# Kernel optimization log

Hardware: AMD Instinct MI355X
Metric: run time of the kernel (lower is better)

The kernel has to match this reference:

```python
import jax, jax.numpy as jnp
import numpy as np

B, L, D = 4096, 50, 64
NU, NI, NR = 100000, 100000, 5


def setup_inputs() -> dict:
    key = jax.random.key(0)
    ks = jax.random.split(key, 16)
    s = 0.02
    inp = {
        "nodes_v": jax.random.randint(ks[0], (B,), 0, NI),
        "neigh_u": jax.random.randint(ks[1], (B, L), 0, NU),
        "neigh_r": jax.random.randint(ks[2], (B, L), 0, NR),
        "embed_u": jax.random.normal(ks[3], (NU, D)) * s,
        "embed_i": jax.random.normal(ks[4], (NI, D)) * s,
        "embed_r": jax.random.normal(ks[5], (NR, D)) * s,
        # gv MLP: Linear(2D,D) ReLU Linear(D,D) ReLU Linear(D,D)
        "gv_w1": jax.random.normal(ks[6], (2 * D, D)) * s, "gv_b1": jnp.zeros((D,)),
        "gv_w2": jax.random.normal(ks[7], (D, D)) * s,     "gv_b2": jnp.zeros((D,)),
        "gv_w3": jax.random.normal(ks[8], (D, D)) * s,     "gv_b3": jnp.zeros((D,)),
        # attention MLP: Linear(2D,D) ReLU Linear(D,D) ReLU Linear(D,1), softmax over neighbors
        "att_w1": jax.random.normal(ks[9], (2 * D, D)) * s, "att_b1": jnp.zeros((D,)),
        "att_w2": jax.random.normal(ks[10], (D, D)) * s,    "att_b2": jnp.zeros((D,)),
        "att_w3": jax.random.normal(ks[11], (D, 1)) * s,    "att_b3": jnp.zeros((1,)),
        # combine: Linear(2D,D) ReLU Linear(D,D) ReLU
        "wr1_w": jax.random.normal(ks[12], (2 * D, D)) * s, "wr1_b": jnp.zeros((D,)),
        "wr2_w": jax.random.normal(ks[13], (D, D)) * s,     "wr2_b": jnp.zeros((D,)),
    }
    return inp


def reference(nodes_v, neigh_u, neigh_r, embed_u, embed_i, embed_r,
              gv_w1, gv_b1, gv_w2, gv_b2, gv_w3, gv_b3,
              att_w1, att_b1, att_w2, att_b2, att_w3, att_b3,
              wr1_w, wr1_b, wr2_w, wr2_b):
    qj = embed_i[nodes_v]            # [B, D] item reps
    pt = embed_u[neigh_u]            # [B, L, D] neighbor user reps
    er = embed_r[neigh_r]            # [B, L, D] rating reps
    # fusion MLP g(.)
    x = jnp.concatenate([pt, er], axis=-1)                    # [B, L, 2D]
    h = jax.nn.relu(x @ gv_w1 + gv_b1)
    h = jax.nn.relu(h @ gv_w2 + gv_b2)
    fjt = h @ gv_w3 + gv_b3                                   # [B, L, D]
    # attention over neighbors (dropout is identity in eval mode)
    q_rep = jnp.broadcast_to(qj[:, None, :], fjt.shape)       # [B, L, D]
    a = jnp.concatenate([fjt, q_rep], axis=-1)                # [B, L, 2D]
    a = jax.nn.relu(a @ att_w1 + att_b1)
    a = jax.nn.relu(a @ att_w2 + att_b2)
    scores = (a @ att_w3 + att_b3)[..., 0]                    # [B, L]
    mu = jax.nn.softmax(scores, axis=1)                       # softmax over neighbors
    zj = jnp.einsum("bld,bl->bd", fjt, mu)                   # weighted aggregation
    # combine aggregated neighborhood with item's own embedding (2D -> D)
    z = jax.nn.relu(jnp.concatenate([zj, qj], axis=-1) @ wr1_w + wr1_b)
    out = jax.nn.relu(z @ wr2_w + wr2_b)                      # [B, D]
    return out
```

## Files before the change

kernel.cpp:

```cpp
#include <hip/hip_runtime.h>

typedef __bf16 bf16;
typedef short s16x8 __attribute__((ext_vector_type(8)));
typedef __bf16 b16x8 __attribute__((ext_vector_type(8)));
typedef float f32x4 __attribute__((ext_vector_type(4)));

#define B_   4096
#define L_   50
#define NROW (B_ * L_)
#define SX   136

#define OFF_W1T  0
#define OFF_W2T  8192
#define OFF_W3T  12288
#define OFF_WCA  16384
#define OFF_A2T  20480
#define OFF_R1T  24576
#define OFF_R2T  32768
#define WT_TOTAL 36864
#define BIAS1P_BYTE 73728
#define C_BYTE      73984
#define SC_BYTE     1122560
#define FJ_BYTE     1941760

__device__ __forceinline__ unsigned short f2b(float f) {
    __bf16 h = (__bf16)f;
    return __builtin_bit_cast(unsigned short, h);
}
__device__ __forceinline__ unsigned pack2(float a, float b) {
    return (unsigned)f2b(a) | ((unsigned)f2b(b) << 16);
}
__device__ __forceinline__ int div50(int x) {
    return (int)(((unsigned long long)(unsigned)x * 2748779070ull) >> 37);
}

template<int KT, bool RELU>
__device__ __forceinline__ void dual_layer(const bf16* A0, const bf16* A1,
                                           const bf16* Wp, const float* __restrict__ bias,
                                           bf16* O0, bf16* O1, int lane)
{
    const int m = lane & 15, quad = lane >> 4;
    f32x4 ac0[4] = {}, ac1[4] = {};
#pragma unroll
    for (int kt = 0; kt < KT; ++kt) {
        s16x8 a0 = *(const s16x8*)(A0 + m * SX + kt * 32 + quad * 8);
        s16x8 a1 = *(const s16x8*)(A1 + m * SX + kt * 32 + quad * 8);
#pragma unroll
        for (int nt = 0; nt < 4; ++nt) {
            s16x8 b = *(const s16x8*)(Wp + (nt * 16 + m) * (KT * 32) + kt * 32 + quad * 8);
            ac0[nt] = __builtin_amdgcn_mfma_f32_16x16x32_bf16(a0, b, ac0[nt], 0, 0, 0);
            ac1[nt] = __builtin_amdgcn_mfma_f32_16x16x32_bf16(a1, b, ac1[nt], 0, 0, 0);
        }
    }
#pragma unroll
    for (int nt = 0; nt < 4; ++nt) {
        int c = nt * 16 + m;
        float bv = bias[c];
#pragma unroll
        for (int r4 = 0; r4 < 4; ++r4) {
            float v0 = ac0[nt][r4] + bv, v1 = ac1[nt][r4] + bv;
            if (RELU) { v0 = fmaxf(v0, 0.f); v1 = fmaxf(v1, 0.f); }
            O0[(quad * 4 + r4) * SX + c] = (bf16)v0;
            O1[(quad * 4 + r4) * SX + c] = (bf16)v1;
        }
    }
}

extern "C" __global__ void prep_weights(const float* __restrict__ w1, const float* __restrict__ w2,
                                        const float* __restrict__ w3, const float* __restrict__ a1,
                                        const float* __restrict__ a2, const float* __restrict__ r1,
                                        const float* __restrict__ r2, const float* __restrict__ gb3,
                                        const float* __restrict__ ab1,
                                        bf16* __restrict__ wt, float* __restrict__ bias1p)
{
    int i = blockIdx.x * blockDim.x + threadIdx.x;
    if (i >= WT_TOTAL + 64) return;
    if (i >= WT_TOTAL) {
        int n = i - WT_TOTAL;
        float s0 = ab1[n], s1 = 0.f, s2 = 0.f, s3 = 0.f;
#pragma unroll
        for (int t = 0; t < 64; t += 4) {
            s0 = fmaf(gb3[t],     a1[t * 64 + n],       s0);
            s1 = fmaf(gb3[t + 1], a1[(t + 1) * 64 + n], s1);
            s2 = fmaf(gb3[t + 2], a1[(t + 2) * 64 + n], s2);
            s3 = fmaf(gb3[t + 3], a1[(t + 3) * 64 + n], s3);
        }
        bias1p[n] = (s0 + s1) + (s2 + s3);
        return;
    }
    float val;
    if (i < OFF_W2T)      { int li = i;            int n = li >> 7, k = li & 127; val = w1[k * 64 + n]; }
    else if (i < OFF_W3T) { int li = i - OFF_W2T;  int n = li >> 6, k = li & 63;  val = w2[k * 64 + n]; }
    else if (i < OFF_WCA) { int li = i - OFF_W3T;  int n = li >> 6, k = li & 63;  val = w3[k * 64 + n]; }
    else if (i < OFF_A2T) {
        int li = i - OFF_WCA; int n = li >> 6, k = li & 63;
        float s0 = 0.f, s1 = 0.f, s2 = 0.f, s3 = 0.f;
#pragma unroll
        for (int t = 0; t < 64; t += 4) {
            float4 w = *(const float4*)(w3 + k * 64 + t);
            s0 = fmaf(w.x, a1[t * 64 + n],       s0);
            s1 = fmaf(w.y, a1[(t + 1) * 64 + n], s1);
            s2 = fmaf(w.z, a1[(t + 2) * 64 + n], s2);
            s3 = fmaf(w.w, a1[(t + 3) * 64 + n], s3);
        }
        val = (s0 + s1) + (s2 + s3);
    }
    else if (i < OFF_R1T) { int li = i - OFF_A2T;  int n = li >> 6, k = li & 63;  val = a2[k * 64 + n]; }
    else if (i < OFF_R2T) { int li = i - OFF_R1T;  int n = li >> 7, k = li & 127; val = r1[k * 64 + n]; }
    else                  { int li = i - OFF_R2T;  int n = li >> 6, k = li & 63;  val = r2[k * 64 + n]; }
    wt[i] = (bf16)val;
}

extern "C" __global__ void __launch_bounds__(256, 4)
prep_citem(const int* __restrict__ nodes_v, const float* __restrict__ embed_i,
           const float* __restrict__ a1, const float* __restrict__ bias1p,
           float* __restrict__ cft)
{
    int gid = blockIdx.x * blockDim.x + threadIdx.x;
    int b = gid >> 6, n = gid & 63;
    int v = nodes_v[b];
    const float* q = embed_i + v * 64;
    float s0 = bias1p[n], s1 = 0.f, s2 = 0.f, s3 = 0.f;
#pragma unroll
    for (int k = 0; k < 64; k += 4) {
        s0 = fmaf(q[k],     a1[(64 + k) * 64 + n],     s0);
        s1 = fmaf(q[k + 1], a1[(64 + k + 1) * 64 + n], s1);
        s2 = fmaf(q[k + 2], a1[(64 + k + 2) * 64 + n], s2);
        s3 = fmaf(q[k + 3], a1[(64 + k + 3) * 64 + n], s3);
    }
    cft[gid] = (s0 + s1) + (s2 + s3);
}

extern "C" __global__ void __launch_bounds__(256, 2)
dense_fwd(const int* __restrict__ neigh_u, const int* __restrict__ neigh_r,
          const float* __restrict__ embed_u, const float* __restrict__ embed_r,
          const float* __restrict__ gv_b1, const float* __restrict__ gv_b2,
          const float* __restrict__ gv_b3,
          const float* __restrict__ att_b2, const float* __restrict__ att_w3,
          const bf16* __restrict__ wt, const float* __restrict__ cft,
          bf16* __restrict__ fj, float* __restrict__ scg)
{
    __shared__ __align__(16) bf16 Xs[128 * SX];
    __shared__ __align__(16) bf16 Ws[16384];
    __shared__ float csS[4 * 64];

    const int tid = threadIdx.x;
    const int lane = tid & 63, wave = tid >> 6;
    const int m = lane & 15, quad = lane >> 4;
    const int r0 = blockIdx.x * 128;
    const int b0 = div50(r0);

    {
        const uint4* src = (const uint4*)(wt + OFF_W2T);
        uint4* dst = (uint4*)Ws;
#pragma unroll
        for (int it = 0; it < 8; ++it) dst[tid + it * 256] = src[tid + it * 256];
    }
    {
        int i = tid >> 6, n = tid & 63;
        int bi = b0 + i; if (bi > B_ - 1) bi = B_ - 1;
        csS[tid] = cft[bi * 64 + n];
    }

    const int rw0 = wave * 32;
    {
        const int rsub = lane >> 4;
        const int c = lane & 15;
#pragma unroll
        for (int it = 0; it < 8; ++it) {
            int rloc = rw0 + it * 4 + rsub;
            int rg = r0 + rloc;
            int u = neigh_u[rg];
            int r = neigh_r[rg];
            float4 vu = *(const float4*)(embed_u + u * 64 + c * 4);
            float4 vr = *(const float4*)(embed_r + r * 64 + c * 4);
            uint2 pu, pr;
            pu.x = pack2(vu.x, vu.y); pu.y = pack2(vu.z, vu.w);
            pr.x = pack2(vr.x, vr.y); pr.y = pack2(vr.z, vr.w);
            *(uint2*)(Xs + rloc * SX + c * 4) = pu;
            *(uint2*)(Xs + rloc * SX + 64 + c * 4) = pr;
        }
    }

    bf16* X0 = Xs + rw0 * SX;
    bf16* X1 = Xs + (rw0 + 16) * SX;

    dual_layer<4, true>(X0, X1, wt + OFF_W1T, gv_b1, X0 + 64, X1 + 64, lane);

    __syncthreads();

    dual_layer<2, true>(X0 + 64, X1 + 64, Ws, gv_b2, X0, X1, lane);

    {
        const bf16* w3s = Ws + 4096;
        const bf16* wcs = Ws + 8192;
        f32x4 aF0[4] = {}, aF1[4] = {}, aA0[4] = {}, aA1[4] = {};
#pragma unroll
        for (int kt = 0; kt < 2; ++kt) {
            s16x8 a0 = *(const s16x8*)(X0 + m * SX + kt * 32 + quad * 8);
            s16x8 a1 = *(const s16x8*)(X1 + m * SX + kt * 32 + quad * 8);
#pragma unroll
            for (int nt = 0; nt < 4; ++nt) {
                s16x8 bF = *(const s16x8*)(w3s + (nt * 16 + m) * 64 + kt * 32 + quad * 8);
                s16x8 bA = *(const s16x8*)(wcs + (nt * 16 + m) * 64 + kt * 32 + quad * 8);
                aF0[nt] = __builtin_amdgcn_mfma_f32_16x16x32_bf16(a0, bF, aF0[nt], 0, 0, 0);
                aF1[nt] = __builtin_amdgcn_mfma_f32_16x16x32_bf16(a1, bF, aF1[nt], 0, 0, 0);
                aA0[nt] = __builtin_amdgcn_mfma_f32_16x16x32_bf16(a0, bA, aA0[nt], 0, 0, 0);
                aA1[nt] = __builtin_amdgcn_mfma_f32_16x16x32_bf16(a1, bA, aA1[nt], 0, 0, 0);
            }
        }
#pragma unroll
        for (int nt = 0; nt < 4; ++nt) {
            int c = nt * 16 + m;
            float b3v = gv_b3[c];
#pragma unroll
            for (int r4 = 0; r4 < 4; ++r4) {
                int rl0 = rw0 + quad * 4 + r4, rl1 = rl0 + 16;
                int i0 = div50(r0 + rl0) - b0, i1 = div50(r0 + rl1) - b0;
                Xs[rl0 * SX + 64 + c] = (bf16)(aF0[nt][r4] + b3v);
                Xs[rl1 * SX + 64 + c] = (bf16)(aF1[nt][r4] + b3v);
                Xs[rl0 * SX + c] = (bf16)fmaxf(aA0[nt][r4] + csS[i0 * 64 + c], 0.f);
                Xs[rl1 * SX + c] = (bf16)fmaxf(aA1[nt][r4] + csS[i1 * 64 + c], 0.f);
            }
        }
    }

    {
        const bf16* a2s = Ws + 12288;
        f32x4 ac0[4] = {}, ac1[4] = {};
#pragma unroll
        for (int kt = 0; kt < 2; ++kt) {
            s16x8 a0 = *(const s16x8*)(X0 + m * SX + kt * 32 + quad * 8);
            s16x8 a1 = *(const s16x8*)(X1 + m * SX + kt * 32 + quad * 8);
#pragma unroll
            for (int nt = 0; nt < 4; ++nt) {
                s16x8 b = *(const s16x8*)(a2s + (nt * 16 + m) * 64 + kt * 32 + quad * 8);
                ac0[nt] = __builtin_amdgcn_mfma_f32_16x16x32_bf16(a0, b, ac0[nt], 0, 0, 0);
                ac1[nt] = __builtin_amdgcn_mfma_f32_16x16x32_bf16(a1, b, ac1[nt], 0, 0, 0);
            }
        }
        float s0[4] = {0.f, 0.f, 0.f, 0.f}, s1[4] = {0.f, 0.f, 0.f, 0.f};
#pragma unroll
        for (int nt = 0; nt < 4; ++nt) {
            int c = nt * 16 + m;
            float b2v = att_b2[c], w3v = att_w3[c];
#pragma unroll
            for (int r4 = 0; r4 < 4; ++r4) {
                s0[r4] += fmaxf(ac0[nt][r4] + b2v, 0.f) * w3v;
                s1[r4] += fmaxf(ac1[nt][r4] + b2v, 0.f) * w3v;
            }
        }
#pragma unroll
        for (int mask = 1; mask < 16; mask <<= 1)
#pragma unroll
            for (int r4 = 0; r4 < 4; ++r4) {
                s0[r4] += __shfl_xor(s0[r4], mask);
                s1[r4] += __shfl_xor(s1[r4], mask);
            }
        if (m == 0) {
#pragma unroll
            for (int r4 = 0; r4 < 4; ++r4) {
                scg[r0 + rw0 + quad * 4 + r4] = s0[r4];
                scg[r0 + rw0 + 16 + quad * 4 + r4] = s1[r4];
            }
        }
    }

    {
        const int rsub = lane >> 3;
        const int ch = lane & 7;
#pragma unroll
        for (int it = 0; it < 4; ++it) {
            int rloc = rw0 + it * 8 + rsub;
            *(uint4*)(fj + (r0 + rloc) * 64 + ch * 8) =
                *(const uint4*)(Xs + rloc * SX + 64 + ch * 8);
        }
    }
}

extern "C" __global__ void __launch_bounds__(256, 4)
aggregate(const int* __restrict__ nodes_v, const float* __restrict__ embed_i,
          const float* __restrict__ scg, const bf16* __restrict__ fj,
          const float* __restrict__ wr1_b, const float* __restrict__ wr2_b,
          const bf16* __restrict__ wt, float* __restrict__ out)
{
    __shared__ float qsh[4][64];
    __shared__ float zsh[4][64];
    __shared__ float z2sh[4][64];

    const int tid = threadIdx.x;
    const int lane = tid & 63, wave = tid >> 6;
    const int b = blockIdx.x * 4 + wave;
    const int d = lane;

    float s = (lane < L_) ? scg[b * L_ + lane] : -1e30f;
    float mx = s;
#pragma unroll
    for (int off = 32; off; off >>= 1) mx = fmaxf(mx, __shfl_xor(mx, off));
    float e = (lane < L_) ? __expf(s - mx) : 0.f;
    float sum = e;
#pragma unroll
    for (int off = 32; off; off >>= 1) sum += __shfl_xor(sum, off);
    float mu = e / sum;

    const bf16* fb = fj + b * L_ * 64;
    float z = 0.f;
#pragma unroll
    for (int l = 0; l < L_; ++l)
        z += (float)fb[l * 64 + d] * __shfl(mu, l);
    zsh[wave][d] = z;
    int v = nodes_v[b];
    qsh[wave][d] = embed_i[v * 64 + d];

    float accz = wr1_b[d];
    const bf16* r1 = wt + OFF_R1T + d * 128;
#pragma unroll
    for (int k8 = 0; k8 < 8; ++k8) {
        b16x8 wv = *(const b16x8*)(r1 + k8 * 8);
#pragma unroll
        for (int j = 0; j < 8; ++j) accz = fmaf((float)wv[j], zsh[wave][k8 * 8 + j], accz);
    }
#pragma unroll
    for (int k8 = 0; k8 < 8; ++k8) {
        b16x8 wv = *(const b16x8*)(r1 + 64 + k8 * 8);
#pragma unroll
        for (int j = 0; j < 8; ++j) accz = fmaf((float)wv[j], qsh[wave][k8 * 8 + j], accz);
    }
    z2sh[wave][d] = fmaxf(accz, 0.f);

    float acco = wr2_b[d];
    const bf16* r2 = wt + OFF_R2T + d * 64;
#pragma unroll
    for (int k8 = 0; k8 < 8; ++k8) {
        b16x8 wv = *(const b16x8*)(r2 + k8 * 8);
#pragma unroll
        for (int j = 0; j < 8; ++j) acco = fmaf((float)wv[j], z2sh[wave][k8 * 8 + j], acco);
    }
    out[b * 64 + d] = fmaxf(acco, 0.f);
}

extern "C" void kernel_launch(void* const* d_in, const int* in_sizes, int n_in,
                              void* d_out, int out_size, void* d_ws, size_t ws_size,
                              hipStream_t stream)
{
    const int* nodes_v = (const int*)d_in[0];
    const int* neigh_u = (const int*)d_in[1];
    const int* neigh_r = (const int*)d_in[2];
    const float* embed_u = (const float*)d_in[3];
    const float* embed_i = (const float*)d_in[4];
    const float* embed_r = (const float*)d_in[5];
    const float* gv_w1  = (const float*)d_in[6];  const float* gv_b1 = (const float*)d_in[7];
    const float* gv_w2  = (const float*)d_in[8];  const float* gv_b2 = (const float*)d_in[9];
    const float* gv_w3  = (const float*)d_in[10]; const float* gv_b3 = (const float*)d_in[11];
    const float* att_w1 = (const float*)d_in[12]; const float* att_b1 = (const float*)d_in[13];
    const float* att_w2 = (const float*)d_in[14]; const float* att_b2 = (const float*)d_in[15];
    const float* att_w3 = (const float*)d_in[16]; const float* att_b3 = (const float*)d_in[17];
    const float* wr1_w  = (const float*)d_in[18]; const float* wr1_b = (const float*)d_in[19];
    const float* wr2_w  = (const float*)d_in[20]; const float* wr2_b = (const float*)d_in[21];
    (void)att_b3;

    bf16*  wt     = (bf16*)d_ws;
    float* bias1p = (float*)((char*)d_ws + BIAS1P_BYTE);
    float* cft    = (float*)((char*)d_ws + C_BYTE);
    float* scg    = (float*)((char*)d_ws + SC_BYTE);
    bf16*  fjp    = (bf16*)((char*)d_ws + FJ_BYTE);

    prep_weights<<<(WT_TOTAL + 64 + 255) / 256, 256, 0, stream>>>(
        gv_w1, gv_w2, gv_w3, att_w1, att_w2, wr1_w, wr2_w, gv_b3, att_b1, wt, bias1p);
    prep_citem<<<(B_ * 64) / 256, 256, 0, stream>>>(nodes_v, embed_i, att_w1, bias1p, cft);
    dense_fwd<<<NROW / 128, 256, 0, stream>>>(neigh_u, neigh_r, embed_u, embed_r,
                                              gv_b1, gv_b2, gv_b3, att_b2, att_w3,
                                              wt, cft, fjp, scg);
    aggregate<<<B_ / 4, 256, 0, stream>>>(nodes_v, embed_i, scg, fjp,
                                          wr1_b, wr2_b, wt, (float*)d_out);
}
```

Before: 189.4 us.

## Pre-swizzle MLP weights into MFMA fragment order and read them from global memory

The prep kernel now writes the first five weight matrices in MFMA B-fragment order, so each lane reads one contiguous 16-byte chunk per fragment. The dense kernel no longer stages W2/W3/Wc/A2 into a 32KB shared buffer and loads every B operand straight from global memory (L1/L2-cached). This removes the LDS copy and frees shared memory, which can raise occupancy. In exchange, every MFMA waits on global or cache loads rather than LDS reads.

```diff
diff --git a/kernel.cpp b/kernel.cpp
--- a/kernel.cpp
+++ b/kernel.cpp
@@ -10,11 +10,11 @@
 #define NROW (B_ * L_)
 #define SX   136
 
-#define OFF_W1T  0
-#define OFF_W2T  8192
-#define OFF_W3T  12288
-#define OFF_WCA  16384
-#define OFF_A2T  20480
+#define OFF_W1F  0
+#define OFF_W2F  8192
+#define OFF_W3F  12288
+#define OFF_WCF  16384
+#define OFF_A2F  20480
 #define OFF_R1T  24576
 #define OFF_R2T  32768
 #define WT_TOTAL 36864
@@ -36,7 +36,8 @@
 
 template<int KT, bool RELU>
 __device__ __forceinline__ void dual_layer(const bf16* A0, const bf16* A1,
-                                           const bf16* Wp, const float* __restrict__ bias,
+                                           const bf16* __restrict__ Wf,
+                                           const float* __restrict__ bias,
                                            bf16* O0, bf16* O1, int lane)
 {
     const int m = lane & 15, quad = lane >> 4;
@@ -47,7 +48,7 @@
         s16x8 a1 = *(const s16x8*)(A1 + m * SX + kt * 32 + quad * 8);
 #pragma unroll
         for (int nt = 0; nt < 4; ++nt) {
-            s16x8 b = *(const s16x8*)(Wp + (nt * 16 + m) * (KT * 32) + kt * 32 + quad * 8);
+            s16x8 b = *(const s16x8*)(Wf + (kt * 4 + nt) * 512 + lane * 8);
             ac0[nt] = __builtin_amdgcn_mfma_f32_16x16x32_bf16(a0, b, ac0[nt], 0, 0, 0);
             ac1[nt] = __builtin_amdgcn_mfma_f32_16x16x32_bf16(a1, b, ac1[nt], 0, 0, 0);
         }
@@ -89,25 +90,37 @@
         return;
     }
     float val;
-    if (i < OFF_W2T)      { int li = i;            int n = li >> 7, k = li & 127; val = w1[k * 64 + n]; }
-    else if (i < OFF_W3T) { int li = i - OFF_W2T;  int n = li >> 6, k = li & 63;  val = w2[k * 64 + n]; }
-    else if (i < OFF_WCA) { int li = i - OFF_W3T;  int n = li >> 6, k = li & 63;  val = w3[k * 64 + n]; }
-    else if (i < OFF_A2T) {
-        int li = i - OFF_WCA; int n = li >> 6, k = li & 63;
-        float s0 = 0.f, s1 = 0.f, s2 = 0.f, s3 = 0.f;
-#pragma unroll
-        for (int t = 0; t < 64; t += 4) {
-            float4 w = *(const float4*)(w3 + k * 64 + t);
-            s0 = fmaf(w.x, a1[t * 64 + n],       s0);
-            s1 = fmaf(w.y, a1[(t + 1) * 64 + n], s1);
-            s2 = fmaf(w.z, a1[(t + 2) * 64 + n], s2);
-            s3 = fmaf(w.w, a1[(t + 3) * 64 + n], s3);
-        }
-        val = (s0 + s1) + (s2 + s3);
-    }
-    else if (i < OFF_R1T) { int li = i - OFF_A2T;  int n = li >> 6, k = li & 63;  val = a2[k * 64 + n]; }
-    else if (i < OFF_R2T) { int li = i - OFF_R1T;  int n = li >> 7, k = li & 127; val = r1[k * 64 + n]; }
-    else                  { int li = i - OFF_R2T;  int n = li >> 6, k = li & 63;  val = r2[k * 64 + n]; }
+    if (i < OFF_R1T) {
+        int off, kind;
+        if      (i < OFF_W2F) { off = OFF_W1F; kind = 0; }
+        else if (i < OFF_W3F) { off = OFF_W2F; kind = 1; }
+        else if (i < OFF_WCF) { off = OFF_W3F; kind = 2; }
+        else if (i < OFF_A2F) { off = OFF_WCF; kind = 3; }
+        else                  { off = OFF_A2F; kind = 4; }
+        int local = i - off;
+        int f = local >> 9, lane = (local >> 3) & 63, j = local & 7;
+        int kt = f >> 2, nt = f & 3, quad = lane >> 4, m = lane & 15;
+        int k = kt * 32 + quad * 8 + j;
+        int n = nt * 16 + m;
+        if (kind == 0)      val = w1[k * 64 + n];
+        else if (kind == 1) val = w2[k * 64 + n];
+        else if (kind == 2) val = w3[k * 64 + n];
+        else if (kind == 4) val = a2[k * 64 + n];
+        else {
+            float s0 = 0.f, s1 = 0.f, s2 = 0.f, s3 = 0.f;
+#pragma unroll
+            for (int t = 0; t < 64; t += 4) {
+                float4 w = *(const float4*)(w3 + k * 64 + t);
+                s0 = fmaf(w.x, a1[t * 64 + n],       s0);
+                s1 = fmaf(w.y, a1[(t + 1) * 64 + n], s1);
+                s2 = fmaf(w.z, a1[(t + 2) * 64 + n], s2);
+                s3 = fmaf(w.w, a1[(t + 3) * 64 + n], s3);
+            }
+            val = (s0 + s1) + (s2 + s3);
+        }
+    }
+    else if (i < OFF_R2T) { int li = i - OFF_R1T; int n = li >> 7, k = li & 127; val = r1[k * 64 + n]; }
+    else                  { int li = i - OFF_R2T; int n = li >> 6, k = li & 63;  val = r2[k * 64 + n]; }
     wt[i] = (bf16)val;
 }
 
@@ -141,7 +154,6 @@
           bf16* __restrict__ fj, float* __restrict__ scg)
 {
     __shared__ __align__(16) bf16 Xs[128 * SX];
-    __shared__ __align__(16) bf16 Ws[16384];
     __shared__ float csS[4 * 64];
 
     const int tid = threadIdx.x;
@@ -150,12 +162,6 @@
     const int r0 = blockIdx.x * 128;
     const int b0 = div50(r0);
 
-    {
-        const uint4* src = (const uint4*)(wt + OFF_W2T);
-        uint4* dst = (uint4*)Ws;
-#pragma unroll
-        for (int it = 0; it < 8; ++it) dst[tid + it * 256] = src[tid + it * 256];
-    }
     {
         int i = tid >> 6, n = tid & 63;
         int bi = b0 + i; if (bi > B_ - 1) bi = B_ - 1;
@@ -185,15 +191,15 @@
     bf16* X0 = Xs + rw0 * SX;
     bf16* X1 = Xs + (rw0 + 16) * SX;
 
-    dual_layer<4, true>(X0, X1, wt + OFF_W1T, gv_b1, X0 + 64, X1 + 64, lane);
+    dual_layer<4, true>(X0, X1, wt + OFF_W1F, gv_b1, X0 + 64, X1 + 64, lane);
 
     __syncthreads();
 
-    dual_layer<2, true>(X0 + 64, X1 + 64, Ws, gv_b2, X0, X1, lane);
-
-    {
-        const bf16* w3s = Ws + 4096;
-        const bf16* wcs = Ws + 8192;
+    dual_layer<2, true>(X0 + 64, X1 + 64, wt + OFF_W2F, gv_b2, X0, X1, lane);
+
+    {
+        const bf16* w3f = wt + OFF_W3F;
+        const bf16* wcf = wt + OFF_WCF;
         f32x4 aF0[4] = {}, aF1[4] = {}, aA0[4] = {}, aA1[4] = {};
 #pragma unroll
         for (int kt = 0; kt < 2; ++kt) {
@@ -201,8 +207,8 @@
             s16x8 a1 = *(const s16x8*)(X1 + m * SX + kt * 32 + quad * 8);
 #pragma unroll
             for (int nt = 0; nt < 4; ++nt) {
-                s16x8 bF = *(const s16x8*)(w3s + (nt * 16 + m) * 64 + kt * 32 + quad * 8);
-                s16x8 bA = *(const s16x8*)(wcs + (nt * 16 + m) * 64 + kt * 32 + quad * 8);
+                s16x8 bF = *(const s16x8*)(w3f + (kt * 4 + nt) * 512 + lane * 8);
+                s16x8 bA = *(const s16x8*)(wcf + (kt * 4 + nt) * 512 + lane * 8);
                 aF0[nt] = __builtin_amdgcn_mfma_f32_16x16x32_bf16(a0, bF, aF0[nt], 0, 0, 0);
                 aF1[nt] = __builtin_amdgcn_mfma_f32_16x16x32_bf16(a1, bF, aF1[nt], 0, 0, 0);
                 aA0[nt] = __builtin_amdgcn_mfma_f32_16x16x32_bf16(a0, bA, aA0[nt], 0, 0, 0);
@@ -226,7 +232,7 @@
     }
 
     {
-        const bf16* a2s = Ws + 12288;
+        const bf16* a2f = wt + OFF_A2F;
         f32x4 ac0[4] = {}, ac1[4] = {};
 #pragma unroll
         for (int kt = 0; kt < 2; ++kt) {
@@ -234,7 +240,7 @@
             s16x8 a1 = *(const s16x8*)(X1 + m * SX + kt * 32 + quad * 8);
 #pragma unroll
             for (int nt = 0; nt < 4; ++nt) {
-                s16x8 b = *(const s16x8*)(a2s + (nt * 16 + m) * 64 + kt * 32 + quad * 8);
+                s16x8 b = *(const s16x8*)(a2f + (kt * 4 + nt) * 512 + lane * 8);
                 ac0[nt] = __builtin_amdgcn_mfma_f32_16x16x32_bf16(a0, b, ac0[nt], 0, 0, 0);
                 ac1[nt] = __builtin_amdgcn_mfma_f32_16x16x32_bf16(a1, b, ac1[nt], 0, 0, 0);
             }
```

Result: faster. 172.2 us (-9.1%).
